# Performance work log

Hardware: AMD Instinct MI355X
Metric: run time of the kernel (lower is better)

The kernel has to match this reference:

```python
import jax, jax.numpy as jnp
import numpy as np

NEG = -1e9  # finite stand-in for -inf so vjp stays NaN-free
BLANK = 28


def setup_inputs() -> dict:
    key = jax.random.key(0)
    k = jax.random.split(key, 6)
    B, T, D, V, L = 64, 1000, 512, 29, 200
    features = jax.random.normal(k[0], (B, T, D), jnp.float32)
    W = jax.random.normal(k[1], (D, V), jnp.float32) / np.sqrt(D)
    b = jnp.zeros((V,), jnp.float32)
    labels = jax.random.randint(k[2], (B, L), 0, BLANK)          # targets never use blank id
    feature_lengths = jax.random.randint(k[3], (B,), T // 2, T + 1)
    label_lengths = jax.random.randint(k[4], (B,), 50, L + 1)
    return dict(features=features, W=W, b=b, labels=labels,
                feature_lengths=feature_lengths, label_lengths=label_lengths)


def _ctc_loss(log_probs, labels, feature_lengths, label_lengths):
    # log_probs: [T, B, V] (already log_softmax'd)
    T, B, V = log_probs.shape
    L = labels.shape[1]
    S = 2 * L + 1  # extended label length (blanks interleaved)
    ext = jnp.full((B, S), BLANK, labels.dtype).at[:, 1::2].set(labels)  # [B,S]
    # skip transition s-2 -> s allowed iff ext[s] != blank and ext[s] != ext[s-2]
    ext_m2 = jnp.pad(ext[:, :-2], ((0, 0), (2, 0)), constant_values=BLANK)
    allow_skip = (ext != BLANK) & (ext != ext_m2)  # [B,S]
    # gather per-timestep log-probs of extended labels: [T,B,S]
    lp_ext = jnp.take_along_axis(log_probs, jnp.broadcast_to(ext[None], (T, B, S)), axis=2)
    # alpha trellis, t = 0
    alpha = (jnp.full((B, S), NEG, log_probs.dtype)
             .at[:, 0].set(lp_ext[0, :, 0])
             .at[:, 1].set(lp_ext[0, :, 1]))

    def step(alpha, inp):
        lp_t, t = inp  # lp_t: [B,S]
        a2 = jnp.pad(alpha[:, :-1], ((0, 0), (1, 0)), constant_values=NEG)
        a3 = jnp.where(allow_skip,
                       jnp.pad(alpha[:, :-2], ((0, 0), (2, 0)), constant_values=NEG),
                       NEG)
        new = lp_t + jnp.logaddexp(jnp.logaddexp(alpha, a2), a3)
        # freeze alpha once past this sample's input length
        new = jnp.where(t < feature_lengths[:, None], new, alpha)
        return new, None

    alpha, _ = jax.lax.scan(step, alpha, (lp_ext[1:], jnp.arange(1, T)))
    # final states: last blank (2*L_b) and last label (2*L_b - 1)
    idx_blank = 2 * label_lengths  # [B]
    l1 = jnp.take_along_axis(alpha, idx_blank[:, None], axis=1)[:, 0]
    l2 = jnp.take_along_axis(alpha, jnp.maximum(idx_blank - 1, 0)[:, None], axis=1)[:, 0]
    l2 = jnp.where(label_lengths > 0, l2, NEG)
    nll = -jnp.logaddexp(l1, l2)  # [B]
    # PyTorch reduction='mean': divide each loss by target length, then average.
    # zero_infinity=True: infeasible (effectively infinite) losses are zeroed.
    denom = jnp.maximum(label_lengths, 1).astype(log_probs.dtype)
    nll = jnp.where(nll < -0.5 * NEG, nll / denom, 0.0)
    return jnp.mean(nll)


def reference(features, W, b, labels, feature_lengths, label_lengths):
    # model head: Linear(D -> V), then log_softmax and (B,T,V) -> (T,B,V)
    logits = jnp.einsum('btd,dv->btv', features, W) + b
    log_probs = jax.nn.log_softmax(logits, axis=-1).transpose(1, 0, 2)
    return _ctc_loss(log_probs, labels, feature_lengths, label_lengths)
```

## Files before the change

kernel.cpp:

```cpp
#include <hip/hip_runtime.h>
#include <hip/hip_bf16.h>
#include <math.h>

#define B_  64
#define T_  1000
#define D_  512
#define V_  29
#define L_  200
#define S_  401
#define VPAD 32
#define BLANK_ 28

__global__ __launch_bounds__(256) void head_softmax_kernel(
    const float* __restrict__ feat,
    const float* __restrict__ W,
    const float* __restrict__ bias,
    const int*   __restrict__ flen,
    float*       __restrict__ p)
{
    __shared__ float frow[8][D_];
    const int g    = threadIdx.x >> 5;
    const int lane = threadIdx.x & 31;
    const int r    = blockIdx.x * 8 + g;
    const int b    = r / T_;
    const int t    = r - b * T_;
    const bool active = (t < flen[b]);

    if (active) {
        const float4* src = (const float4*)(feat + (size_t)r * D_);
        float4* dst = (float4*)frow[g];
        #pragma unroll
        for (int i = 0; i < 4; ++i) dst[lane + 32 * i] = src[lane + 32 * i];
    }
    __syncthreads();

    if (active) {
        float logit = -1e30f;
        if (lane < V_) {
            float a0 = bias[lane], a1 = 0.f, a2 = 0.f, a3 = 0.f;
            const float* w = W + lane;
            #pragma unroll 8
            for (int d = 0; d < D_; d += 4) {
                a0 += frow[g][d]     * w[(size_t)d * V_];
                a1 += frow[g][d + 1] * w[(size_t)(d + 1) * V_];
                a2 += frow[g][d + 2] * w[(size_t)(d + 2) * V_];
                a3 += frow[g][d + 3] * w[(size_t)(d + 3) * V_];
            }
            logit = (a0 + a1) + (a2 + a3);
        }
        float mx = logit;
        #pragma unroll
        for (int off = 16; off; off >>= 1)
            mx = fmaxf(mx, __shfl_xor(mx, off, 32));
        float e = (lane < V_) ? __expf(logit - mx) : 0.f;
        float se = e;
        #pragma unroll
        for (int off = 16; off; off >>= 1)
            se += __shfl_xor(se, off, 32);
        p[(size_t)r * VPAD + lane] = (lane < V_) ? e / se : 0.f;
    }
}

__device__ __forceinline__ float wave_shr1_zero(float x) {
    return __int_as_float(__builtin_amdgcn_update_dpp(
        0, __float_as_int(x), 0x138 , 0xf, 0xf, true));
}
__device__ __forceinline__ int shr1_self_i(int x) {
    return __builtin_amdgcn_update_dpp(x, x, 0x138 , 0xf, 0xf, false);
}

#define TWO60  1.152921504606846976e18f
#define TWOM60 8.673617379884035e-19f
#define NEGLOG2 (-1.5e9f)

#define CTC_STEP(Q) do {                                                      \
    int   cp = shr1_self_i(c);                                                \
    float u1 = wave_shr1_zero(r[6]);                                          \
    float u2 = wave_shr1_zero(r[5]);                                          \
    int   cm = (c > cp) ? c : cp;                                             \
    int   dc = c  - cm; if (dc < -127) dc = -127;                             \
    int   dp = cp - cm; if (dp < -127) dp = -127;                             \
    float fs = __int_as_float((dc + 127) << 23);                              \
    float fu = __int_as_float((dp + 127) << 23);                              \
    u1 *= fu; u2 *= fu;                                                       \
    float s0 = r[0]*fs, s1 = r[1]*fs, s2 = r[2]*fs, s3 = r[3]*fs;             \
    float s4 = r[4]*fs, s5 = r[5]*fs, s6 = r[6]*fs;                           \
    float n0 = Q[0] * (s0 + u1 + allowf[0] * u2);                             \
    float n1 = Q[1] * (s1 + s0 + allowf[1] * u1);                             \
    float n2 = Q[2] * (s2 + s1 + allowf[2] * s0);                             \
    float n3 = Q[3] * (s3 + s2 + allowf[3] * s1);                             \
    float n4 = Q[4] * (s4 + s3 + allowf[4] * s2);                             \
    float n5 = Q[5] * (s5 + s4 + allowf[5] * s3);                             \
    float n6 = Q[6] * (s6 + s5 + allowf[6] * s4);                             \
    float m  = fmaxf(fmaxf(fmaxf(n0, n1), fmaxf(n2, n3)),                     \
                     fmaxf(fmaxf(n4, n5), n6));                               \
    m = fmaxf(m, TWOM60);                                                     \
    int e   = (__float_as_int(m) >> 23) - 127;            \
    float sc = __int_as_float((187 - e) << 23);          \
    r[0]=n0*sc; r[1]=n1*sc; r[2]=n2*sc; r[3]=n3*sc;                           \
    r[4]=n4*sc; r[5]=n5*sc; r[6]=n6*sc;                                       \
    c = cm + e - 60;                                                          \
} while (0)

#define PREFETCH(Q, row) do {                                                 \
    int _base = (row) * VPAD;                                                 \
    Q[0]=plds[_base+oi[0]]; Q[1]=plds[_base+oi[1]]; Q[2]=plds[_base+oi[2]];   \
    Q[3]=plds[_base+oi[3]]; Q[4]=plds[_base+oi[4]]; Q[5]=plds[_base+oi[5]];   \
    Q[6]=plds[_base+oi[6]];                                                   \
} while (0)

__global__ __launch_bounds__(256) void ctc_alpha_lds_kernel(
    const float* __restrict__ p,
    const int*   __restrict__ labels,
    const int*   __restrict__ flen,
    const int*   __restrict__ llen,
    float*       __restrict__ nll)
{
    __shared__ float plds[T_ * VPAD];
    const int b   = blockIdx.x;
    const int tid = threadIdx.x;
    const float* pb = p + (size_t)b * T_ * VPAD;
    const int Tb = flen[b];
    const int ll = llen[b];

    {
        const float4* src4 = (const float4*)pb;
        float4* dst4 = (float4*)plds;
        const int n4 = Tb * (VPAD / 4);
        for (int i = tid; i < n4; i += 256) dst4[i] = src4[i];
    }
    __syncthreads();

    if (tid < 64) {
        const int lane = tid;

        int   oi[7];
        float allowf[7];
        #pragma unroll
        for (int k = 0; k < 7; ++k) {
            int s = 7 * lane + k;
            int o = 29;
            float al = 0.f;
            if (s < S_) {
                if (s & 1) {
                    int li = (s - 1) >> 1;
                    o = labels[b * L_ + li];
                    if (s >= 3) al = (o != labels[b * L_ + li - 1]) ? 1.f : 0.f;
                } else {
                    o = BLANK_;
                }
            }
            oi[k]     = o;
            allowf[k] = al;
        }

        float r[7];
        int   c = -60;
        {
            float q0[7];
            PREFETCH(q0, 0);
            #pragma unroll
            for (int k = 0; k < 7; ++k)
                r[k] = (lane == 0 && k < 2) ? q0[k] * TWO60 : 0.f;
        }

        float qA[7], qB[7], qN1[7], qN2[7];
        PREFETCH(qA, 1);
        PREFETCH(qB, 2);
        const int Tbm1 = Tb - 1;

        int t = 1;
        for (; t + 1 < Tb; t += 2) {
            int rowA = t + 2; if (rowA > Tbm1) rowA = Tbm1;
            int rowB = t + 3; if (rowB > Tbm1) rowB = Tbm1;
            PREFETCH(qN1, rowA);
            CTC_STEP(qA);
            PREFETCH(qN2, rowB);
            CTC_STEP(qB);
            #pragma unroll
            for (int k = 0; k < 7; ++k) { qA[k] = qN1[k]; qB[k] = qN2[k]; }
        }
        if (t < Tb) CTC_STEP(qA);

        #pragma unroll
        for (int k = 0; k < 7; ++k) {
            float v = r[k];
            plds[7 * lane + k] = (v > 0.f) ? ((float)c + log2f(v)) : NEGLOG2;
        }
    }
    __syncthreads();

    if (tid == 0) {
        int ib = 2 * ll;
        float l1 = plds[ib];
        float l2 = (ll > 0) ? plds[ib - 1] : NEGLOG2;
        float mm = fmaxf(l1, l2);
        float s2 = exp2f(l1 - mm) + exp2f(l2 - mm);
        float nl = -0.6931471805599453f * (mm + log2f(s2));
        nll[b] = (nl < 5e8f) ? nl / fmaxf((float)ll, 1.f) : 0.f;
    }
}

__global__ __launch_bounds__(64) void reduce_mean_kernel(
    const float* __restrict__ nll, float* __restrict__ out)
{
    float v = nll[threadIdx.x];
    #pragma unroll
    for (int off = 32; off; off >>= 1) v += __shfl_down(v, off);
    if (threadIdx.x == 0) out[0] = v * (1.0f / (float)B_);
}

extern "C" void kernel_launch(void* const* d_in, const int* in_sizes, int n_in,
                              void* d_out, int out_size, void* d_ws, size_t ws_size,
                              hipStream_t stream) {
    const float* feat   = (const float*)d_in[0];
    const float* W      = (const float*)d_in[1];
    const float* bias   = (const float*)d_in[2];
    const int*   labels = (const int*)  d_in[3];
    const int*   flen   = (const int*)  d_in[4];
    const int*   llen   = (const int*)  d_in[5];
    float* out = (float*)d_out;

    float* p   = (float*)d_ws;
    float* nll = (float*)((char*)d_ws + (size_t)8 * 1024 * 1024);

    head_softmax_kernel<<<(B_ * T_) / 8, 256, 0, stream>>>(feat, W, bias, flen, p);
    ctc_alpha_lds_kernel<<<B_, 256, 0, stream>>>(p, labels, flen, llen, nll);
    reduce_mean_kernel<<<1, 64, 0, stream>>>(nll, out);
}
```

Before: 426.3 us.

## Compute linear head with bf16 MFMA tiles and fused softmax

Replaces the scalar per-row dot-product head with a 16x16x32 bf16 MFMA kernel. W is converted to bf16 fragments in LDS once per block, and each wave processes two 16-row tiles, converting features to bf16 on the fly. Softmax is done on the accumulator layout with 16-lane shuffles. The aim is to cut the FMA-bound head GEMM cost, at the price of bf16 rounding of features and weights, which could change the loss slightly.

```diff
diff --git a/kernel.cpp b/kernel.cpp
--- a/kernel.cpp
+++ b/kernel.cpp
@@ -11,53 +11,102 @@
 #define VPAD 32
 #define BLANK_ 28
 
-__global__ __launch_bounds__(256) void head_softmax_kernel(
+typedef __attribute__((ext_vector_type(8))) short short8v;
+typedef __attribute__((ext_vector_type(4))) float float4v;
+
+__device__ __forceinline__ unsigned short f2bf(float f) {
+    unsigned int u = __float_as_uint(f);
+    return (unsigned short)((u + 0x7FFFu + ((u >> 16) & 1u)) >> 16);
+}
+
+__global__ __launch_bounds__(256) void head_mfma_softmax_kernel(
     const float* __restrict__ feat,
     const float* __restrict__ W,
     const float* __restrict__ bias,
     const int*   __restrict__ flen,
     float*       __restrict__ p)
 {
-    __shared__ float frow[8][D_];
-    const int g    = threadIdx.x >> 5;
-    const int lane = threadIdx.x & 31;
-    const int r    = blockIdx.x * 8 + g;
-    const int b    = r / T_;
-    const int t    = r - b * T_;
-    const bool active = (t < flen[b]);
-
-    if (active) {
-        const float4* src = (const float4*)(feat + (size_t)r * D_);
-        float4* dst = (float4*)frow[g];
-        #pragma unroll
-        for (int i = 0; i < 4; ++i) dst[lane + 32 * i] = src[lane + 32 * i];
+    __shared__ uint4 bfrag_lds[16 * 2 * 64];
+    const int tid = threadIdx.x;
+
+    for (int f = tid; f < 2048; f += 256) {
+        int ks  = f >> 7;
+        int rem = f & 127;
+        int tl  = rem >> 6;
+        int ln  = rem & 63;
+        int k0  = ks * 32 + (ln >> 4) * 8;
+        int col = tl * 16 + (ln & 15);
+        unsigned short h[8];
+        #pragma unroll
+        for (int j = 0; j < 8; ++j) {
+            float wv = (col < V_) ? W[(size_t)(k0 + j) * V_ + col] : 0.f;
+            h[j] = f2bf(wv);
+        }
+        uint4 pk;
+        pk.x = h[0] | ((unsigned)h[1] << 16);
+        pk.y = h[2] | ((unsigned)h[3] << 16);
+        pk.z = h[4] | ((unsigned)h[5] << 16);
+        pk.w = h[6] | ((unsigned)h[7] << 16);
+        bfrag_lds[f] = pk;
     }
     __syncthreads();
 
-    if (active) {
-        float logit = -1e30f;
-        if (lane < V_) {
-            float a0 = bias[lane], a1 = 0.f, a2 = 0.f, a3 = 0.f;
-            const float* w = W + lane;
-            #pragma unroll 8
-            for (int d = 0; d < D_; d += 4) {
-                a0 += frow[g][d]     * w[(size_t)d * V_];
-                a1 += frow[g][d + 1] * w[(size_t)(d + 1) * V_];
-                a2 += frow[g][d + 2] * w[(size_t)(d + 2) * V_];
-                a3 += frow[g][d + 3] * w[(size_t)(d + 3) * V_];
-            }
-            logit = (a0 + a1) + (a2 + a3);
-        }
-        float mx = logit;
-        #pragma unroll
-        for (int off = 16; off; off >>= 1)
-            mx = fmaxf(mx, __shfl_xor(mx, off, 32));
-        float e = (lane < V_) ? __expf(logit - mx) : 0.f;
-        float se = e;
-        #pragma unroll
-        for (int off = 16; off; off >>= 1)
-            se += __shfl_xor(se, off, 32);
-        p[(size_t)r * VPAD + lane] = (lane < V_) ? e / se : 0.f;
+    const int wv  = tid >> 6;
+    const int l   = tid & 63;
+    const int c0  = l & 15;
+    const int grp = l >> 4;
+    const float bias0 = bias[c0];
+    const bool  v1ok  = (c0 + 16) < V_;
+    const float bias1 = v1ok ? bias[c0 + 16] : 0.f;
+
+    #pragma unroll
+    for (int ti = 0; ti < 2; ++ti) {
+        const int tile = (blockIdx.x * 4 + wv) * 2 + ti;
+        const int r0   = tile * 16;
+        const int b0 = r0 / T_;
+        const bool active = ((r0 - b0 * T_) < flen[b0]) || ((r0 + 15) / T_ != b0);
+        if (!active) continue;
+
+        const float* abase = feat + (size_t)(r0 + c0) * D_ + grp * 8;
+        float4v acc0 = {0.f, 0.f, 0.f, 0.f};
+        float4v acc1 = {0.f, 0.f, 0.f, 0.f};
+
+        #pragma unroll 4
+        for (int ks = 0; ks < 16; ++ks) {
+            float4 fa = *(const float4*)(abase + ks * 32);
+            float4 fb = *(const float4*)(abase + ks * 32 + 4);
+            short8v a;
+            a[0] = (short)f2bf(fa.x); a[1] = (short)f2bf(fa.y);
+            a[2] = (short)f2bf(fa.z); a[3] = (short)f2bf(fa.w);
+            a[4] = (short)f2bf(fb.x); a[5] = (short)f2bf(fb.y);
+            a[6] = (short)f2bf(fb.z); a[7] = (short)f2bf(fb.w);
+            uint4 b0v = bfrag_lds[(ks * 2 + 0) * 64 + l];
+            uint4 b1v = bfrag_lds[(ks * 2 + 1) * 64 + l];
+            acc0 = __builtin_amdgcn_mfma_f32_16x16x32_bf16(
+                       a, __builtin_bit_cast(short8v, b0v), acc0, 0, 0, 0);
+            acc1 = __builtin_amdgcn_mfma_f32_16x16x32_bf16(
+                       a, __builtin_bit_cast(short8v, b1v), acc1, 0, 0, 0);
+        }
+
+        #pragma unroll
+        for (int j = 0; j < 4; ++j) {
+            float lg0 = acc0[j] + bias0;
+            float lg1 = v1ok ? (acc1[j] + bias1) : -1e30f;
+            float m = fmaxf(lg0, lg1);
+            #pragma unroll
+            for (int off = 1; off <= 8; off <<= 1)
+                m = fmaxf(m, __shfl_xor(m, off));
+            float e0 = __expf(lg0 - m);
+            float e1 = v1ok ? __expf(lg1 - m) : 0.f;
+            float s = e0 + e1;
+            #pragma unroll
+            for (int off = 1; off <= 8; off <<= 1)
+                s += __shfl_xor(s, off);
+            float invs = 1.f / s;
+            int r = r0 + grp * 4 + j;
+            p[(size_t)r * VPAD + c0]      = e0 * invs;
+            p[(size_t)r * VPAD + c0 + 16] = e1 * invs;
+        }
     }
 }
 
@@ -224,7 +273,7 @@
     float* p   = (float*)d_ws;
     float* nll = (float*)((char*)d_ws + (size_t)8 * 1024 * 1024);
 
-    head_softmax_kernel<<<(B_ * T_) / 8, 256, 0, stream>>>(feat, W, bias, flen, p);
+    head_mfma_softmax_kernel<<<500, 256, 0, stream>>>(feat, W, bias, flen, p);
     ctc_alpha_lds_kernel<<<B_, 256, 0, stream>>>(p, labels, flen, llen, nll);
     reduce_mean_kernel<<<1, 64, 0, stream>>>(nll, out);
 }
```

New measurement: 361.4 us. 15.2% less time.
